# Kernel optimization log

Hardware: AMD Instinct MI355X
Metric: run time of the kernel (lower is better)

## Reference

```python
import jax, jax.numpy as jnp
import numpy as np

B, V, D, H, E = 512, 128, 256, 4, 2
Dh = D // H

def setup_inputs() -> dict:
    key = jax.random.key(0)
    k = jax.random.split(key, 8)
    x = jax.random.normal(k[0], (B, V, D), dtype=jnp.float32)
    adj = jax.random.randint(k[1], (V, V), 0, 2, dtype=jnp.int32)
    adj = adj.at[jnp.arange(V), jnp.arange(V)].set(1)  # self loops so no empty columns for real nodes
    edge_attr = jax.random.normal(k[2], (V, V, E), dtype=jnp.float32)
    mask = jax.random.bernoulli(k[3], 0.1, (B, V))  # True = padded view
    # learned params (torch Linear: y = x @ W.T)
    W = jax.random.normal(k[4], (D, D), dtype=jnp.float32) / np.sqrt(D)
    a = jax.random.normal(k[5], (2 * Dh,), dtype=jnp.float32) / np.sqrt(2 * Dh)  # attn.weight flattened
    Ew = jax.random.normal(k[6], (H, E), dtype=jnp.float32) / np.sqrt(E)  # edge_proj.weight
    return {"x": x, "adj": adj, "edge_attr": edge_attr, "mask": mask, "W": W, "a": a, "Ew": Ew}

def reference(x, adj, edge_attr, mask, W, a, Ew):
    Bv, Vv, Dv = x.shape
    Hh = Ew.shape[0]
    Dhh = Dv // Hh
    Wx = (x @ W.T).reshape(Bv, Vv, Hh, Dhh)                 # [B,V,H,Dh]
    a_src, a_dst = a[:Dhh], a[Dhh:]
    s_src = jnp.einsum('bvhd,d->bvh', Wx, a_src)             # a^T[Wh_i ; .]
    s_dst = jnp.einsum('bvhd,d->bvh', Wx, a_dst)             # a^T[. ; Wh_j]
    ef = jnp.einsum('ije,he->ijh', edge_attr, Ew)            # [V,V,H]
    e = s_src[:, :, None, :] + s_dst[:, None, :, :] + ef[None]  # [B,i,j,H]
    e = jnp.where(e >= 0, e, 0.2 * e)                        # leaky_relu(0.2)
    valid = (adj.astype(bool))[None, :, :, None] & (~mask)[:, :, None, None] & (~mask)[:, None, :, None]
    e = jnp.where(valid, e, -jnp.inf)
    # softmax over source dim i (axis=1), safe for all-masked columns (-> 0, like nan_to_num)
    m = jnp.max(e, axis=1, keepdims=True)
    m = jnp.where(jnp.isfinite(m), m, 0.0)
    p = jnp.where(valid, jnp.exp(e - m), 0.0)
    denom = jnp.sum(p, axis=1, keepdims=True)
    alpha = p / jnp.where(denom == 0, 1.0, denom)            # [B,i,j,H]
    h = jnp.einsum('bijh,bihd->bjhd', alpha, Wx).reshape(Bv, Vv, Dv)
    h = jax.nn.elu(h)
    return jnp.where(mask[:, :, None], 0.0, h)
```

## Files before the change

### kernel.cpp

```cpp
#include <hip/hip_runtime.h>
#include <hip/hip_bf16.h>
#include <cmath>

#define BB 512
#define VV 128
#define DD 256
#define HH 4
#define DHH 64

typedef unsigned short u16;
typedef __attribute__((ext_vector_type(8))) short bf16x8;
typedef __attribute__((ext_vector_type(4))) short bf16x4;
typedef __attribute__((ext_vector_type(4))) float f32x4;

__device__ __forceinline__ unsigned pk2(float a, float b) {
    __hip_bfloat162 h = __float22bfloat162_rn(make_float2(a, b));
    unsigned r;
    __builtin_memcpy(&r, &h, sizeof(r));
    return r;
}

__global__ __launch_bounds__(256) void k_ef(const float* __restrict__ ea,
                                            const float* __restrict__ Ew,
                                            const int* __restrict__ adj,
                                            float* __restrict__ efmT) {
    __shared__ float tile[32][33];
    const int jt = blockIdx.x, it = blockIdx.y, h = blockIdx.z;
    const int t = threadIdx.x;
    const float e0 = Ew[h * 2], e1 = Ew[h * 2 + 1];
    const int jl = t & 31, il = t >> 5;
    #pragma unroll
    for (int p = 0; p < 4; ++p) {
        const int i = it * 32 + p * 8 + il;
        const int j = jt * 32 + jl;
        const int ij = i * VV + j;
        float v = -INFINITY;
        if (adj[ij]) v = fmaf(ea[ij * 2 + 1], e1, ea[ij * 2] * e0);
        tile[p * 8 + il][jl] = v;
    }
    __syncthreads();
    const int i2 = t & 31, j2 = t >> 5;
    #pragma unroll
    for (int p = 0; p < 4; ++p) {
        const int j = p * 8 + j2;
        efmT[((size_t)h * VV + jt * 32 + j) * VV + it * 32 + i2] = tile[i2][j];
    }
}

__global__ __launch_bounds__(256, 4) void k_fused(
    const float* __restrict__ x, const float* __restrict__ Wm,
    const float* __restrict__ a, const float* __restrict__ efmT,
    const int* __restrict__ mask, float* __restrict__ out) {
    __shared__ u16 ubuf[128 * 136];
    __shared__ float ssl[256], sdl[256], rden[2][128];
    __shared__ int mkl[128];

    u16* As  = ubuf;
    u16* Bs  = ubuf + 128 * 40;
    u16* WxL = ubuf;

    const int t = threadIdx.x;
    const int b = blockIdx.x, hp = blockIdx.y;
    const int w = t >> 6, L = t & 63;
    const int wr = w >> 1, wc = w & 1;
    const int lr = L & 15, lg = L >> 4;

    if (t < 128) mkl[t] = mask[b * VV + t];

    const int r0 = t >> 3, c8 = t & 7;
    const float* xs = x  + ((size_t)b * VV + r0) * DD + c8 * 4;
    const float* ws = Wm + ((size_t)(hp * 128 + r0)) * DD + c8 * 4;
    u16* adst = As + r0 * 40 + c8 * 4;
    u16* bdst = Bs + r0 * 40 + c8 * 4;

    f32x4 acc[4][4];
    #pragma unroll
    for (int i = 0; i < 4; ++i)
        #pragma unroll
        for (int j = 0; j < 4; ++j) acc[i][j] = (f32x4){0.f, 0.f, 0.f, 0.f};

    float4 px[4], pw[4];
    #pragma unroll
    for (int q = 0; q < 4; ++q) {
        px[q] = *(const float4*)(xs + (size_t)q * 32 * DD);
        pw[q] = *(const float4*)(ws + (size_t)q * 32 * DD);
    }

    for (int ks = 0; ks < 8; ++ks) {
        #pragma unroll
        for (int q = 0; q < 4; ++q) {
            uint2 ua, ub;
            ua.x = pk2(px[q].x, px[q].y); ua.y = pk2(px[q].z, px[q].w);
            ub.x = pk2(pw[q].x, pw[q].y); ub.y = pk2(pw[q].z, pw[q].w);
            *(uint2*)(adst + q * 32 * 40) = ua;
            *(uint2*)(bdst + q * 32 * 40) = ub;
        }
        __syncthreads();
        if (ks < 7) {
            #pragma unroll
            for (int q = 0; q < 4; ++q) {
                px[q] = *(const float4*)(xs + (size_t)q * 32 * DD + (ks + 1) * 32);
                pw[q] = *(const float4*)(ws + (size_t)q * 32 * DD + (ks + 1) * 32);
            }
        }
        bf16x8 af[4], bfr[4];
        #pragma unroll
        for (int mi = 0; mi < 4; ++mi)
            af[mi] = *(const bf16x8*)&As[(wr * 64 + mi * 16 + lr) * 40 + lg * 8];
        #pragma unroll
        for (int ni = 0; ni < 4; ++ni)
            bfr[ni] = *(const bf16x8*)&Bs[(wc * 64 + ni * 16 + lr) * 40 + lg * 8];
        #pragma unroll
        for (int mi = 0; mi < 4; ++mi)
            #pragma unroll
            for (int ni = 0; ni < 4; ++ni)
                acc[mi][ni] = __builtin_amdgcn_mfma_f32_16x16x32_bf16(
                    af[mi], bfr[ni], acc[mi][ni], 0, 0, 0);
        __syncthreads();
    }

    float as_[4], ad_[4];
    #pragma unroll
    for (int ni = 0; ni < 4; ++ni) {
        as_[ni] = a[ni * 16 + lr];
        ad_[ni] = a[64 + ni * 16 + lr];
    }
    float ps[16], pd[16];
    #pragma unroll
    for (int k = 0; k < 16; ++k) { ps[k] = 0.f; pd[k] = 0.f; }
    #pragma unroll
    for (int mi = 0; mi < 4; ++mi) {
        #pragma unroll
        for (int ni = 0; ni < 4; ++ni) {
            const int c  = wc * 64 + ni * 16 + lr;
            const int vb = wr * 64 + mi * 16 + lg * 4;
            unsigned o2[2];
            o2[0] = pk2(acc[mi][ni][0], acc[mi][ni][1]);
            o2[1] = pk2(acc[mi][ni][2], acc[mi][ni][3]);
            #pragma unroll
            for (int r = 0; r < 4; ++r) {
                float v = acc[mi][ni][r];
                ps[mi * 4 + r] = fmaf(v, as_[ni], ps[mi * 4 + r]);
                pd[mi * 4 + r] = fmaf(v, ad_[ni], pd[mi * 4 + r]);
            }
            *(uint2*)&WxL[c * 136 + vb] = *(uint2*)&o2[0];
        }
    }
    #pragma unroll
    for (int k = 0; k < 16; ++k) {
        #pragma unroll
        for (int m = 1; m < 16; m <<= 1) {
            ps[k] += __shfl_xor(ps[k], m);
            pd[k] += __shfl_xor(pd[k], m);
        }
    }
    if (lr == 0) {
        #pragma unroll
        for (int mi = 0; mi < 4; ++mi)
            #pragma unroll
            for (int r = 0; r < 4; ++r) {
                int v = wr * 64 + mi * 16 + lg * 4 + r;
                bool mk = mkl[v] != 0;
                ssl[wc * 128 + v] = mk ? -INFINITY : ps[mi * 4 + r];
                sdl[wc * 128 + v] = mk ? -INFINITY : pd[mi * 4 + r];
            }
    }
    __syncthreads();

    const int j0 = w * 32 + lr;
    for (int hl = 0; hl < 2; ++hl) {
        const int h = hp * 2 + hl;
        const float sdj0 = sdl[hl * 128 + j0];
        const float sdj1 = sdl[hl * 128 + j0 + 16];
        const float* ef0 = efmT + ((size_t)h * VV + j0) * VV;
        const float* ef1 = ef0 + 16 * VV;
        bf16x8 af2[2][4];
        float ps0 = 0.f, ps1 = 0.f;
        #pragma unroll
        for (int ks = 0; ks < 4; ++ks) {
            const int i0 = ks * 32 + lg * 8;
            float sv[8], ev0[8], ev1[8];
            *(float4*)&sv[0]  = *(const float4*)&ssl[hl * 128 + i0];
            *(float4*)&sv[4]  = *(const float4*)&ssl[hl * 128 + i0 + 4];
            *(float4*)&ev0[0] = *(const float4*)(ef0 + i0);
            *(float4*)&ev0[4] = *(const float4*)(ef0 + i0 + 4);
            *(float4*)&ev1[0] = *(const float4*)(ef1 + i0);
            *(float4*)&ev1[4] = *(const float4*)(ef1 + i0 + 4);
            float p0[8], p1[8];
            #pragma unroll
            for (int u = 0; u < 8; ++u) {
                float e0 = sv[u] + sdj0 + ev0[u];
                float e1 = sv[u] + sdj1 + ev1[u];
                e0 = fmaxf(e0, 0.2f * e0);
                e1 = fmaxf(e1, 0.2f * e1);
                p0[u] = __expf(e0); ps0 += p0[u];
                p1[u] = __expf(e1); ps1 += p1[u];
            }
            unsigned* a0 = (unsigned*)&af2[0][ks];
            unsigned* a1 = (unsigned*)&af2[1][ks];
            a0[0] = pk2(p0[0], p0[1]); a0[1] = pk2(p0[2], p0[3]);
            a0[2] = pk2(p0[4], p0[5]); a0[3] = pk2(p0[6], p0[7]);
            a1[0] = pk2(p1[0], p1[1]); a1[1] = pk2(p1[2], p1[3]);
            a1[2] = pk2(p1[4], p1[5]); a1[3] = pk2(p1[6], p1[7]);
        }
        ps0 += __shfl_xor(ps0, 16); ps0 += __shfl_xor(ps0, 32);
        ps1 += __shfl_xor(ps1, 16); ps1 += __shfl_xor(ps1, 32);
        if (lg == 0) {
            rden[hl][j0]      = ps0 > 0.f ? 1.f / ps0 : 0.f;
            rden[hl][j0 + 16] = ps1 > 0.f ? 1.f / ps1 : 0.f;
        }

        f32x4 acc2[2][4];
        #pragma unroll
        for (int mi = 0; mi < 2; ++mi)
            #pragma unroll
            for (int ni = 0; ni < 4; ++ni) acc2[mi][ni] = (f32x4){0.f, 0.f, 0.f, 0.f};
        #pragma unroll
        for (int ks = 0; ks < 4; ++ks) {
            const int kk = ks * 32 + lg * 8;
            #pragma unroll
            for (int ni = 0; ni < 4; ++ni) {
                bf16x8 bf2 = *(const bf16x8*)&WxL[(hl * 64 + ni * 16 + lr) * 136 + kk];
                acc2[0][ni] = __builtin_amdgcn_mfma_f32_16x16x32_bf16(
                    af2[0][ks], bf2, acc2[0][ni], 0, 0, 0);
                acc2[1][ni] = __builtin_amdgcn_mfma_f32_16x16x32_bf16(
                    af2[1][ks], bf2, acc2[1][ni], 0, 0, 0);
            }
        }
        __syncthreads();

        #pragma unroll
        for (int mi = 0; mi < 2; ++mi)
            #pragma unroll
            for (int ni = 0; ni < 4; ++ni) {
                const int dcol = ni * 16 + lr;
                const int jb   = w * 32 + mi * 16 + lg * 4;
                float* op = out + ((size_t)b * VV + jb) * DD + h * DHH + dcol;
                #pragma unroll
                for (int r = 0; r < 4; ++r) {
                    float v = acc2[mi][ni][r] * rden[hl][jb + r];
                    v = v > 0.f ? v : (__expf(v) - 1.0f);
                    op[(size_t)r * DD] = v;
                }
            }
    }
}

extern "C" void kernel_launch(void* const* d_in, const int* in_sizes, int n_in,
                              void* d_out, int out_size, void* d_ws, size_t ws_size,
                              hipStream_t stream) {
    const float* x    = (const float*)d_in[0];
    const int*   adj  = (const int*)d_in[1];
    const float* ea   = (const float*)d_in[2];
    const int*   mask = (const int*)d_in[3];
    const float* Wm   = (const float*)d_in[4];
    const float* a    = (const float*)d_in[5];
    const float* Ew   = (const float*)d_in[6];
    float* out = (float*)d_out;

    float* efmT = (float*)d_ws;

    k_ef<<<dim3(4, 4, HH), 256, 0, stream>>>(ea, Ew, adj, efmT);
    k_fused<<<dim3(BB, 2), 256, 0, stream>>>(x, Wm, a, efmT, mask, out);
}
```

Measured before the change: 155.9 us.

## Load GEMM fragments directly from global into registers, dropping LDS staging

```diff
diff --git a/kernel.cpp b/kernel.cpp
--- a/kernel.cpp
+++ b/kernel.cpp
@@ -10,7 +10,6 @@
 
 typedef unsigned short u16;
 typedef __attribute__((ext_vector_type(8))) short bf16x8;
-typedef __attribute__((ext_vector_type(4))) short bf16x4;
 typedef __attribute__((ext_vector_type(4))) float f32x4;
 
 __device__ __forceinline__ unsigned pk2(float a, float b) {
@@ -47,17 +46,12 @@
     }
 }
 
-__global__ __launch_bounds__(256, 4) void k_fused(
+__global__ __launch_bounds__(256, 3) void k_fused(
     const float* __restrict__ x, const float* __restrict__ Wm,
     const float* __restrict__ a, const float* __restrict__ efmT,
     const int* __restrict__ mask, float* __restrict__ out) {
-    __shared__ u16 ubuf[128 * 136];
+    __shared__ u16 WxL[128 * 136];
     __shared__ float ssl[256], sdl[256], rden[2][128];
-    __shared__ int mkl[128];
-
-    u16* As  = ubuf;
-    u16* Bs  = ubuf + 128 * 40;
-    u16* WxL = ubuf;
 
     const int t = threadIdx.x;
     const int b = blockIdx.x, hp = blockIdx.y;
@@ -65,13 +59,8 @@
     const int wr = w >> 1, wc = w & 1;
     const int lr = L & 15, lg = L >> 4;
 
-    if (t < 128) mkl[t] = mask[b * VV + t];
-
-    const int r0 = t >> 3, c8 = t & 7;
-    const float* xs = x  + ((size_t)b * VV + r0) * DD + c8 * 4;
-    const float* ws = Wm + ((size_t)(hp * 128 + r0)) * DD + c8 * 4;
-    u16* adst = As + r0 * 40 + c8 * 4;
-    u16* bdst = Bs + r0 * 40 + c8 * 4;
+    const float* xb = x  + ((size_t)b * VV + wr * 64 + lr) * DD + lg * 8;
+    const float* wb = Wm + ((size_t)(hp * 128 + wc * 64 + lr)) * DD + lg * 8;
 
     f32x4 acc[4][4];
     #pragma unroll
@@ -79,44 +68,34 @@
         #pragma unroll
         for (int j = 0; j < 4; ++j) acc[i][j] = (f32x4){0.f, 0.f, 0.f, 0.f};
 
-    float4 px[4], pw[4];
-    #pragma unroll
-    for (int q = 0; q < 4; ++q) {
-        px[q] = *(const float4*)(xs + (size_t)q * 32 * DD);
-        pw[q] = *(const float4*)(ws + (size_t)q * 32 * DD);
-    }
-
     for (int ks = 0; ks < 8; ++ks) {
-        #pragma unroll
-        for (int q = 0; q < 4; ++q) {
-            uint2 ua, ub;
-            ua.x = pk2(px[q].x, px[q].y); ua.y = pk2(px[q].z, px[q].w);
-            ub.x = pk2(pw[q].x, pw[q].y); ub.y = pk2(pw[q].z, pw[q].w);
-            *(uint2*)(adst + q * 32 * 40) = ua;
-            *(uint2*)(bdst + q * 32 * 40) = ub;
-        }
-        __syncthreads();
-        if (ks < 7) {
-            #pragma unroll
-            for (int q = 0; q < 4; ++q) {
-                px[q] = *(const float4*)(xs + (size_t)q * 32 * DD + (ks + 1) * 32);
-                pw[q] = *(const float4*)(ws + (size_t)q * 32 * DD + (ks + 1) * 32);
-            }
-        }
-        bf16x8 af[4], bfr[4];
-        #pragma unroll
-        for (int mi = 0; mi < 4; ++mi)
-            af[mi] = *(const bf16x8*)&As[(wr * 64 + mi * 16 + lr) * 40 + lg * 8];
-        #pragma unroll
-        for (int ni = 0; ni < 4; ++ni)
-            bfr[ni] = *(const bf16x8*)&Bs[(wc * 64 + ni * 16 + lr) * 40 + lg * 8];
+        float4 la[4][2], lb[4][2];
+        #pragma unroll
+        for (int f = 0; f < 4; ++f) {
+            la[f][0] = *(const float4*)(xb + (size_t)f * 16 * DD + ks * 32);
+            la[f][1] = *(const float4*)(xb + (size_t)f * 16 * DD + ks * 32 + 4);
+        }
+        #pragma unroll
+        for (int f = 0; f < 4; ++f) {
+            lb[f][0] = *(const float4*)(wb + (size_t)f * 16 * DD + ks * 32);
+            lb[f][1] = *(const float4*)(wb + (size_t)f * 16 * DD + ks * 32 + 4);
+        }
+        bf16x8 af[4], bf[4];
+        #pragma unroll
+        for (int f = 0; f < 4; ++f) {
+            unsigned* u = (unsigned*)&af[f];
+            u[0] = pk2(la[f][0].x, la[f][0].y); u[1] = pk2(la[f][0].z, la[f][0].w);
+            u[2] = pk2(la[f][1].x, la[f][1].y); u[3] = pk2(la[f][1].z, la[f][1].w);
+            unsigned* v = (unsigned*)&bf[f];
+            v[0] = pk2(lb[f][0].x, lb[f][0].y); v[1] = pk2(lb[f][0].z, lb[f][0].w);
+            v[2] = pk2(lb[f][1].x, lb[f][1].y); v[3] = pk2(lb[f][1].z, lb[f][1].w);
+        }
         #pragma unroll
         for (int mi = 0; mi < 4; ++mi)
             #pragma unroll
             for (int ni = 0; ni < 4; ++ni)
                 acc[mi][ni] = __builtin_amdgcn_mfma_f32_16x16x32_bf16(
-                    af[mi], bfr[ni], acc[mi][ni], 0, 0, 0);
-        __syncthreads();
+                    af[mi], bf[ni], acc[mi][ni], 0, 0, 0);
     }
 
     float as_[4], ad_[4];
@@ -160,7 +139,7 @@
             #pragma unroll
             for (int r = 0; r < 4; ++r) {
                 int v = wr * 64 + mi * 16 + lg * 4 + r;
-                bool mk = mkl[v] != 0;
+                bool mk = mask[b * VV + v] != 0;
                 ssl[wc * 128 + v] = mk ? -INFINITY : ps[mi * 4 + r];
                 sdl[wc * 128 + v] = mk ? -INFINITY : pd[mi * 4 + r];
             }
@@ -227,7 +206,6 @@
                     af2[1][ks], bf2, acc2[1][ni], 0, 0, 0);
             }
         }
-        __syncthreads();
 
         #pragma unroll
         for (int mi = 0; mi < 2; ++mi)
```

After: 182.8 us. 17.2% more time.
